# Kernel optimization log

Hardware: AMD Instinct MI355X
Metric: run time of the kernel (lower is better)

The kernel has to match this reference:

```python
import jax, jax.numpy as jnp
import numpy as np

N_SRC = 20000
N_TAR = 20000
DIM = 3


def setup_inputs() -> dict:
    key = jax.random.key(0)
    k1, k2 = jax.random.split(key)
    src_V = jax.random.normal(k1, (N_SRC, DIM), dtype=jnp.float32)
    tar_V = jax.random.normal(k2, (N_TAR, DIM), dtype=jnp.float32)
    return {"src_V": src_V, "tar_V": tar_V}


def reference(src_V, tar_V):
    # Brute-force 1-NN replacing the CPU cKDTree query.
    # Squared distances: ||t||^2 - 2 t.s^T + ||s||^2  -> [M, N]
    d2 = (
        jnp.sum(tar_V * tar_V, axis=1, keepdims=True)
        - 2.0 * (tar_V @ src_V.T)
        + jnp.sum(src_V * src_V, axis=1)[None, :]
    )
    ii = jnp.argmin(d2, axis=1)          # nearest src index per tar point
    diff = src_V[ii] - tar_V             # gather + residual, [M, 3]
    return 0.5 * jnp.sum(diff * diff)
```

## Files before the change

### kernel.cpp

```cpp
#include <hip/hip_runtime.h>
#include <float.h>

#define N_SRC 20000
#define N_TAR 20000
#define TPB 256
#define SPLITS 16
#define TILES 42
#define PACK_N (SPLITS * TILES * 64)
#define TGRP 79
#define FBLOCKS ((N_TAR + 255) / 256)

typedef _Float16 half8 __attribute__((ext_vector_type(8)));
typedef float floatx16 __attribute__((ext_vector_type(16)));


#define DPP_MIN(v, ctrl) { \
    const int _s = __builtin_amdgcn_update_dpp( \
        __float_as_int(v), __float_as_int(v), (ctrl), 0xf, 0xf, false); \
    v = fminf(v, __int_as_float(_s)); }
#define COL_REDUCE(v) { \
    DPP_MIN(v, 0xB1)   \
    DPP_MIN(v, 0x4E)   \
    DPP_MIN(v, 0x141)  \
    DPP_MIN(v, 0x140)  \
    DPP_MIN(v, 0x142)  }

__global__ __launch_bounds__(TPB) void nn_prep(
    const float* __restrict__ src, half8* __restrict__ pack,
    float* __restrict__ out)
{
    const int i = blockIdx.x * TPB + threadIdx.x;
    if (i == 0) out[0] = 0.f;
    if (i >= PACK_N) return;

    const int L = i & 63;
    const int hf = L >> 5;
    const int s = (i >> 6) * 32 + (L & 31);

    half8 f = {0, 0, 0, 0, 0, 0, 0, 0};
    if (s < N_SRC) {
        const float x = src[s * 3 + 0];
        const float y = src[s * 3 + 1];
        const float z = src[s * 3 + 2];
        const _Float16 xh = (_Float16)x, yh = (_Float16)y, zh = (_Float16)z;
        if (hf == 0) {
            const _Float16 xl = (_Float16)(x - (float)xh);
            const _Float16 yl = (_Float16)(y - (float)yh);
            f = (half8){xh, yh, zh, xh, yh, zh, xl, yl};
        } else {
            const _Float16 zl = (_Float16)(z - (float)zh);
            const float nrm = 0.5f * (x * x + y * y + z * z);
            const _Float16 nh = (_Float16)nrm;
            const _Float16 nl = (_Float16)(nrm - (float)nh);
            f = (half8){zl, nh, nl, 0, 0, 0, 0, 0};
        }
    } else if (hf == 1) {
        f = (half8){0, (_Float16)30000.f, 0, 0, 0, 0, 0, 0};
    }
    pack[i] = f;
}

__global__ __launch_bounds__(TPB, 4) void nn_mfma(
    const half8* __restrict__ pack, const float* __restrict__ tar,
    float* __restrict__ part)
{
    __shared__ half8 lds[TILES * 64];

    const int tid  = threadIdx.x;
    const int lane = tid & 63;
    const int col  = lane & 31;
    const int half = (lane >> 5) & 1;
    const int wave = tid >> 6;

    const half8* gp = pack + (size_t)blockIdx.y * (TILES * 64);
    for (int g = tid; g < TILES * 64; g += TPB) lds[g] = pack[(size_t)blockIdx.y * (TILES * 64) + g];
    (void)gp;

    const int strip0 = (blockIdx.x * 4 + wave) * 2;
    half8 a0, a1;
#pragma unroll
    for (int sidx = 0; sidx < 2; ++sidx) {
        const int t = min((strip0 + sidx) * 32 + col, N_TAR - 1);
        const float tx = tar[t * 3 + 0];
        const float ty = tar[t * 3 + 1];
        const float tz = tar[t * 3 + 2];
        const _Float16 txh = (_Float16)tx, tyh = (_Float16)ty, tzh = (_Float16)tz;
        const _Float16 txl = (_Float16)(tx - (float)txh);
        const _Float16 tyl = (_Float16)(ty - (float)tyh);
        const _Float16 tzl = (_Float16)(tz - (float)tzh);
        half8 a;
        if (half == 0)
            a = (half8){-txh, -tyh, -tzh, -txl, -tyl, -tzl, -txh, -tyh};
        else
            a = (half8){-tzh, (_Float16)1.f, (_Float16)1.f, 0, 0, 0, 0, 0};
        if (sidx == 0) a0 = a; else a1 = a;
    }

    __syncthreads();

    floatx16 m0, m1;
#pragma unroll
    for (int i = 0; i < 16; ++i) { m0[i] = FLT_MAX; m1[i] = FLT_MAX; }
    const floatx16 zero = {};

    const half8* lp = lds + lane;
    half8 r0 = lp[0 * 64];
    half8 r1 = lp[1 * 64];
    half8 r2 = lp[2 * 64];
    half8 r3 = lp[3 * 64];
#pragma unroll 1
    for (int tp = 0; tp < TILES; tp += 2) {
        const int nx = min(tp + 4, TILES - 2);
        const half8 n0 = lp[nx * 64];
        const half8 n1 = lp[nx * 64 + 64];
        {
            const floatx16 d00 = __builtin_amdgcn_mfma_f32_32x32x16_f16(a0, r0, zero, 0, 0, 0);
            const floatx16 d01 = __builtin_amdgcn_mfma_f32_32x32x16_f16(a0, r1, zero, 0, 0, 0);
#pragma unroll
            for (int i = 0; i < 16; ++i) m0[i] = fminf(m0[i], fminf(d00[i], d01[i]));
        }
        {
            const floatx16 d10 = __builtin_amdgcn_mfma_f32_32x32x16_f16(a1, r0, zero, 0, 0, 0);
            const floatx16 d11 = __builtin_amdgcn_mfma_f32_32x32x16_f16(a1, r1, zero, 0, 0, 0);
#pragma unroll
            for (int i = 0; i < 16; ++i) m1[i] = fminf(m1[i], fminf(d10[i], d11[i]));
        }
        r0 = r2; r1 = r3; r2 = n0; r3 = n1;
    }

#pragma unroll
    for (int i = 0; i < 16; ++i) { COL_REDUCE(m0[i]) COL_REDUCE(m1[i]) }

    if (col == 16) {
        float* prow = part + (size_t)blockIdx.y * N_TAR;
#pragma unroll
        for (int i = 0; i < 16; ++i) {
            const int row = (i & 3) + 8 * (i >> 2) + 4 * half;
            const int t0 = min(strip0 * 32 + row, N_TAR - 1);
            const int t1 = min((strip0 + 1) * 32 + row, N_TAR - 1);
            prow[t0] = m0[i];
            prow[t1] = m1[i];
        }
    }
}

__global__ __launch_bounds__(256) void nn_finalize(
    const float* __restrict__ tar, const float* __restrict__ part,
    float* __restrict__ out)
{
    const int t = blockIdx.x * 256 + threadIdx.x;
    float contrib = 0.f;
    if (t < N_TAR) {
        float m = FLT_MAX;
#pragma unroll
        for (int c = 0; c < SPLITS; ++c) m = fminf(m, part[c * N_TAR + t]);
        const float tx = tar[t * 3 + 0];
        const float ty = tar[t * 3 + 1];
        const float tz = tar[t * 3 + 2];
        contrib = 0.5f * (tx * tx + ty * ty + tz * tz) + m;
    }
    for (int off = 32; off > 0; off >>= 1)
        contrib += __shfl_down(contrib, off);
    __shared__ float red[4];
    if ((threadIdx.x & 63) == 0) red[threadIdx.x >> 6] = contrib;
    __syncthreads();
    if (threadIdx.x == 0) {
        float s = 0.f;
#pragma unroll
        for (int w = 0; w < 4; ++w) s += red[w];
        atomicAdd(out, s);
    }
}

extern "C" void kernel_launch(void* const* d_in, const int* in_sizes, int n_in,
                              void* d_out, int out_size, void* d_ws, size_t ws_size,
                              hipStream_t stream) {
    const float* src = (const float*)d_in[0];
    const float* tar = (const float*)d_in[1];
    float* out = (float*)d_out;

    char* w = (char*)d_ws;
    float* part = (float*)w;
    half8* pack = (half8*)(w + 2 * 1024 * 1024);

    nn_prep<<<(PACK_N + TPB - 1) / TPB, TPB, 0, stream>>>(src, pack, out);
    dim3 grid1(TGRP, SPLITS);
    nn_mfma<<<grid1, TPB, 0, stream>>>(pack, tar, part);
    nn_finalize<<<FBLOCKS, 256, 0, stream>>>(tar, part, out);
}
```

Baseline: 89.36 us.

## Process four target strips per wave and read source tiles directly from global

Each wave now computes four 32-row target strips instead of two, so every source tile loaded feeds four MFMA pairs. The grid shrinks from 79 to 40 blocks along x. The LDS staging of the packed source tiles and its barrier are removed, and the waves read tiles straight from global memory through the cache. The cost is more accumulator registers, fewer resident blocks (640 total), and global load latency in the inner loop instead of LDS latency.

```diff
diff --git a/kernel.cpp b/kernel.cpp
--- a/kernel.cpp
+++ b/kernel.cpp
@@ -7,7 +7,7 @@
 #define SPLITS 16
 #define TILES 42
 #define PACK_N (SPLITS * TILES * 64)
-#define TGRP 79
+#define TGRP 40
 #define FBLOCKS ((N_TAR + 255) / 256)
 
 typedef _Float16 half8 __attribute__((ext_vector_type(8)));
@@ -60,87 +60,78 @@
     pack[i] = f;
 }
 
-__global__ __launch_bounds__(TPB, 4) void nn_mfma(
+#define MAKE_A(out_a, sidx) { \
+    const int t = min((strip0 + (sidx)) * 32 + col, N_TAR - 1); \
+    const float tx = tar[t * 3 + 0]; \
+    const float ty = tar[t * 3 + 1]; \
+    const float tz = tar[t * 3 + 2]; \
+    const _Float16 txh = (_Float16)tx, tyh = (_Float16)ty, tzh = (_Float16)tz; \
+    const _Float16 txl = (_Float16)(tx - (float)txh); \
+    const _Float16 tyl = (_Float16)(ty - (float)tyh); \
+    const _Float16 tzl = (_Float16)(tz - (float)tzh); \
+    out_a = (half == 0) \
+        ? (half8){-txh, -tyh, -tzh, -txl, -tyl, -tzl, -txh, -tyh} \
+        : (half8){-tzh, (_Float16)1.f, (_Float16)1.f, 0, 0, 0, 0, 0}; }
+
+#define TILE_STEP(aa, mm, t0_, t1_) { \
+    const floatx16 d0 = __builtin_amdgcn_mfma_f32_32x32x16_f16(aa, t0_, zero, 0, 0, 0); \
+    const floatx16 d1 = __builtin_amdgcn_mfma_f32_32x32x16_f16(aa, t1_, zero, 0, 0, 0); \
+    _Pragma("unroll") \
+    for (int i = 0; i < 16; ++i) mm[i] = fminf(mm[i], fminf(d0[i], d1[i])); }
+
+#define STORE_STRIP(mm, sidx) { \
+    _Pragma("unroll") \
+    for (int i = 0; i < 16; ++i) { \
+        const int row = (i & 3) + 8 * (i >> 2) + 4 * half; \
+        const int t = min((strip0 + (sidx)) * 32 + row, N_TAR - 1); \
+        prow[t] = mm[i]; } }
+
+__global__ __launch_bounds__(TPB) void nn_mfma(
     const half8* __restrict__ pack, const float* __restrict__ tar,
     float* __restrict__ part)
 {
-    __shared__ half8 lds[TILES * 64];
-
     const int tid  = threadIdx.x;
     const int lane = tid & 63;
     const int col  = lane & 31;
     const int half = (lane >> 5) & 1;
     const int wave = tid >> 6;
 
-    const half8* gp = pack + (size_t)blockIdx.y * (TILES * 64);
-    for (int g = tid; g < TILES * 64; g += TPB) lds[g] = pack[(size_t)blockIdx.y * (TILES * 64) + g];
-    (void)gp;
+    const int strip0 = (blockIdx.x * 4 + wave) * 4;
+    half8 a0, a1, a2, a3;
+    MAKE_A(a0, 0) MAKE_A(a1, 1) MAKE_A(a2, 2) MAKE_A(a3, 3)
 
-    const int strip0 = (blockIdx.x * 4 + wave) * 2;
-    half8 a0, a1;
+    const half8* bp = pack + (size_t)blockIdx.y * (TILES * 64) + lane;
+
+    floatx16 m0, m1, m2, m3;
 #pragma unroll
-    for (int sidx = 0; sidx < 2; ++sidx) {
-        const int t = min((strip0 + sidx) * 32 + col, N_TAR - 1);
-        const float tx = tar[t * 3 + 0];
-        const float ty = tar[t * 3 + 1];
-        const float tz = tar[t * 3 + 2];
-        const _Float16 txh = (_Float16)tx, tyh = (_Float16)ty, tzh = (_Float16)tz;
-        const _Float16 txl = (_Float16)(tx - (float)txh);
-        const _Float16 tyl = (_Float16)(ty - (float)tyh);
-        const _Float16 tzl = (_Float16)(tz - (float)tzh);
-        half8 a;
-        if (half == 0)
-            a = (half8){-txh, -tyh, -tzh, -txl, -tyl, -tzl, -txh, -tyh};
-        else
-            a = (half8){-tzh, (_Float16)1.f, (_Float16)1.f, 0, 0, 0, 0, 0};
-        if (sidx == 0) a0 = a; else a1 = a;
-    }
-
-    __syncthreads();
-
-    floatx16 m0, m1;
-#pragma unroll
-    for (int i = 0; i < 16; ++i) { m0[i] = FLT_MAX; m1[i] = FLT_MAX; }
+    for (int i = 0; i < 16; ++i) { m0[i] = FLT_MAX; m1[i] = FLT_MAX;
+                                   m2[i] = FLT_MAX; m3[i] = FLT_MAX; }
     const floatx16 zero = {};
 
-    const half8* lp = lds + lane;
-    half8 r0 = lp[0 * 64];
-    half8 r1 = lp[1 * 64];
-    half8 r2 = lp[2 * 64];
-    half8 r3 = lp[3 * 64];
+    half8 r0 = bp[0 * 64];
+    half8 r1 = bp[1 * 64];
+    half8 r2 = bp[2 * 64];
+    half8 r3 = bp[3 * 64];
 #pragma unroll 1
     for (int tp = 0; tp < TILES; tp += 2) {
         const int nx = min(tp + 4, TILES - 2);
-        const half8 n0 = lp[nx * 64];
-        const half8 n1 = lp[nx * 64 + 64];
-        {
-            const floatx16 d00 = __builtin_amdgcn_mfma_f32_32x32x16_f16(a0, r0, zero, 0, 0, 0);
-            const floatx16 d01 = __builtin_amdgcn_mfma_f32_32x32x16_f16(a0, r1, zero, 0, 0, 0);
-#pragma unroll
-            for (int i = 0; i < 16; ++i) m0[i] = fminf(m0[i], fminf(d00[i], d01[i]));
-        }
-        {
-            const floatx16 d10 = __builtin_amdgcn_mfma_f32_32x32x16_f16(a1, r0, zero, 0, 0, 0);
-            const floatx16 d11 = __builtin_amdgcn_mfma_f32_32x32x16_f16(a1, r1, zero, 0, 0, 0);
-#pragma unroll
-            for (int i = 0; i < 16; ++i) m1[i] = fminf(m1[i], fminf(d10[i], d11[i]));
-        }
+        const half8 n0 = bp[nx * 64];
+        const half8 n1 = bp[nx * 64 + 64];
+        TILE_STEP(a0, m0, r0, r1)
+        TILE_STEP(a1, m1, r0, r1)
+        TILE_STEP(a2, m2, r0, r1)
+        TILE_STEP(a3, m3, r0, r1)
         r0 = r2; r1 = r3; r2 = n0; r3 = n1;
     }
 
 #pragma unroll
-    for (int i = 0; i < 16; ++i) { COL_REDUCE(m0[i]) COL_REDUCE(m1[i]) }
+    for (int i = 0; i < 16; ++i) {
+        COL_REDUCE(m0[i]) COL_REDUCE(m1[i]) COL_REDUCE(m2[i]) COL_REDUCE(m3[i])
+    }
 
     if (col == 16) {
         float* prow = part + (size_t)blockIdx.y * N_TAR;
-#pragma unroll
-        for (int i = 0; i < 16; ++i) {
-            const int row = (i & 3) + 8 * (i >> 2) + 4 * half;
-            const int t0 = min(strip0 * 32 + row, N_TAR - 1);
-            const int t1 = min((strip0 + 1) * 32 + row, N_TAR - 1);
-            prow[t0] = m0[i];
-            prow[t1] = m1[i];
-        }
+        STORE_STRIP(m0, 0) STORE_STRIP(m1, 1) STORE_STRIP(m2, 2) STORE_STRIP(m3, 3)
     }
 }
 
```

Result: no change. 91.01 us (+1.8%).
